# Kernel tuning notes

Hardware: AMD Instinct MI355X
Metric: run time of the kernel (lower is better)

Reference implementation:

```python
import jax, jax.numpy as jnp
import numpy as np

B, C, F = 64, 512, 48
D, H, L, HID = 16, 4, 2, 256   # d_token, n_heads, n_blocks, hidden_dim
DH = D // H
FF = 4 * D
EPS = 1e-5


def _ln(x, s, b):
    m = x.mean(-1, keepdims=True)
    v = x.var(-1, keepdims=True)
    return (x - m) * jax.lax.rsqrt(v + EPS) * s + b


def setup_inputs() -> dict:
    key = jax.random.key(0)
    ks = jax.random.split(key, 10)
    def n(k, shape, s=0.02):
        return jax.random.normal(k, shape, dtype=jnp.float32) * s
    return {
        'couple_features': jax.random.normal(ks[0], (B, F, C), dtype=jnp.float32),
        'feature_embed': n(ks[1], (F, D)),
        'feature_bias': jnp.zeros((F, D), jnp.float32),
        'cls_token': n(ks[2], (D,)),
        'track_embed': n(ks[3], (3, D)),
        'role_ids': jnp.repeat(jnp.arange(3, dtype=jnp.int32), 16),  # [0]*16+[1]*16+[2]*16
        'ln1_s': jnp.ones((L, D), jnp.float32), 'ln1_b': jnp.zeros((L, D), jnp.float32),
        'qkv_w': n(ks[4], (L, D, 3 * D), 0.1), 'qkv_b': jnp.zeros((L, 3 * D), jnp.float32),
        'out_w': n(ks[5], (L, D, D), 0.1), 'out_b': jnp.zeros((L, D), jnp.float32),
        'ln2_s': jnp.ones((L, D), jnp.float32), 'ln2_b': jnp.zeros((L, D), jnp.float32),
        'ff1_w': n(ks[6], (L, D, FF), 0.1), 'ff1_b': jnp.zeros((L, FF), jnp.float32),
        'ff2_w': n(ks[7], (L, FF, D), 0.1), 'ff2_b': jnp.zeros((L, D), jnp.float32),
        'cls2h_w': n(ks[8], (D, HID), 0.1), 'cls2h_b': jnp.zeros((HID,), jnp.float32),
    }


def reference(couple_features, feature_embed, feature_bias, cls_token, track_embed,
              role_ids, ln1_s, ln1_b, qkv_w, qkv_b, out_w, out_b,
              ln2_s, ln2_b, ff1_w, ff1_b, ff2_w, ff2_b, cls2h_w, cls2h_b):
    Bc, Fc, Cc = couple_features.shape
    N, T = Bc * Cc, Fc + 1
    # tokenise: (B,F,C) -> (B*C, F, 1) scalar * per-feature embed + bias + role embed
    scalars = couple_features.transpose(0, 2, 1).reshape(N, Fc, 1)
    tokens = scalars * feature_embed + feature_bias + track_embed[role_ids]
    cls = jnp.broadcast_to(cls_token, (N, 1, D))
    x = jnp.concatenate([cls, tokens], axis=1)  # (N, T, D)
    scale = 1.0 / np.sqrt(DH)
    for l in range(L):  # pre-LN transformer blocks (norm_first=True, gelu)
        h = _ln(x, ln1_s[l], ln1_b[l])
        qkv = h @ qkv_w[l] + qkv_b[l]
        q, k, v = jnp.split(qkv, 3, axis=-1)
        q = q.reshape(N, T, H, DH)
        k = k.reshape(N, T, H, DH)
        v = v.reshape(N, T, H, DH)
        s = jnp.einsum('nqhd,nkhd->nhqk', q, k) * scale
        a = jax.nn.softmax(s, axis=-1)
        ctx = jnp.einsum('nhqk,nkhd->nqhd', a, v).reshape(N, T, D)
        x = x + ctx @ out_w[l] + out_b[l]
        h2 = _ln(x, ln2_s[l], ln2_b[l])
        x = x + jax.nn.gelu(h2 @ ff1_w[l] + ff1_b[l], approximate=False) @ ff2_w[l] + ff2_b[l]
    cls_out = x[:, 0, :]
    out = (cls_out @ cls2h_w + cls2h_b).reshape(Bc, Cc, HID)
    return out.transpose(0, 2, 1)  # (B, hidden_dim, C)
```

## Files before the change

kernel.cpp:

```cpp
#include <hip/hip_runtime.h>
#include <math.h>

#define Bc    64
#define Cc    512
#define Fc    48
#define NTOT  32768
#define TT    49
#define NS    5
#define NBLK  ((NTOT + NS - 1) / NS)
#define QSCALE 0.72134752044448169f
#define GC1 (-2.3022082f)
#define GC2 (-0.10294324f)

#define EXP2(x) __builtin_amdgcn_exp2f(x)
#define RCP(x)  __builtin_amdgcn_rcpf(x)

using h2 = decltype(__builtin_amdgcn_cvt_pkrtz(0.f, 0.f));
typedef _Float16 f16x8 __attribute__((ext_vector_type(8)));
typedef float    f32x4 __attribute__((ext_vector_type(4)));

#define MFMA16(a,b,c) __builtin_amdgcn_mfma_f32_16x16x32_f16((a),(b),(c),0,0,0)

__device__ __forceinline__ h2 PK(float a, float b) {
    return __builtin_amdgcn_cvt_pkrtz(a, b);
}
__device__ __forceinline__ unsigned H2U(h2 h) { return __builtin_bit_cast(unsigned, h); }
__device__ __forceinline__ h2 U2H(unsigned u) { return __builtin_bit_cast(h2, u); }

__device__ __forceinline__ float DOT2(h2 a, h2 b, float c) {
#if __has_builtin(__builtin_amdgcn_fdot2)
    return __builtin_amdgcn_fdot2(a, b, c, false);
#else
    return fmaf((float)a[0], (float)b[0], fmaf((float)a[1], (float)b[1], c));
#endif
}
__device__ __forceinline__ unsigned pack_rte(float a, float b) {
    h2 h; h[0] = (_Float16)a; h[1] = (_Float16)b;
    return __builtin_bit_cast(unsigned, h);
}
__device__ __forceinline__ float gelu1(float g) {
    const float u = g * fmaf(GC2, g * g, GC1);
    return g * RCP(1.0f + EXP2(u));
}

#define OFF_QKVW 0
#define OFF_QKVB 768
#define OFF_OUTW 864
#define OFF_OUTB 1120
#define OFF_C2HW 1152
#define OFF_C2HB 3200
#define OFF_FBTE 3456
#define OFF_F1A  4224
#define OFF_F2A  6272
#define OFF_B1V  7296
#define OFF_B2V  9344
#define WS_DWORDS 9856

__global__ __launch_bounds__(256)
void pack_kernel(const float* __restrict__ qkv_w, const float* __restrict__ qkv_b,
                 const float* __restrict__ out_w, const float* __restrict__ out_b,
                 const float* __restrict__ ff1_w, const float* __restrict__ ff1_b,
                 const float* __restrict__ ff2_w, const float* __restrict__ ff2_b,
                 const float* __restrict__ c2h_w, const float* __restrict__ c2h_b,
                 const float* __restrict__ fb,    const float* __restrict__ te,
                 const int*   __restrict__ role,
                 const float* __restrict__ ln1_s, const float* __restrict__ ln1_b,
                 const float* __restrict__ ln2_s, const float* __restrict__ ln2_b,
                 unsigned* __restrict__ ws)
{
    const int gid = blockIdx.x * 256 + threadIdx.x;
    const int gs  = gridDim.x * 256;
    float* wsf = (float*)ws;
    for (int i = gid; i < 768; i += gs) {
        int dp = i & 7, jl = i >> 3, j = jl % 48, l = jl / 48;
        float w0 = qkv_w[(l*16 + 2*dp    )*48 + j] * ln1_s[l*16 + 2*dp];
        float w1 = qkv_w[(l*16 + 2*dp + 1)*48 + j] * ln1_s[l*16 + 2*dp + 1];
        if (j < 16) { w0 *= QSCALE; w1 *= QSCALE; }
        ws[OFF_QKVW + i] = pack_rte(w0, w1);
    }
    for (int i = gid; i < 96; i += gs) {
        int j = i % 48, l = i / 48;
        float a = qkv_b[i];
        for (int d = 0; d < 16; ++d) a += ln1_b[l*16+d] * qkv_w[(l*16+d)*48 + j];
        wsf[OFF_QKVB + i] = a * (j < 16 ? QSCALE : 1.0f);
    }
    for (int i = gid; i < 256; i += gs) {
        int dp = i & 7, dl = i >> 3, d = dl % 16, l = dl / 16;
        ws[OFF_OUTW + i] = pack_rte(out_w[l*256 + (2*dp)*16 + d],
                                    out_w[l*256 + (2*dp+1)*16 + d]);
    }
    for (int i = gid; i < 32; i += gs) wsf[OFF_OUTB + i] = out_b[i];
    for (int i = gid; i < 2048; i += gs) {
        int dp = i & 7, o = i >> 3;
        ws[OFF_C2HW + i] = pack_rte(c2h_w[(2*dp)*256 + o], c2h_w[(2*dp+1)*256 + o]);
    }
    for (int i = gid; i < 256; i += gs) wsf[OFF_C2HB + i] = c2h_b[i];
    for (int i = gid; i < 768; i += gs) {
        int d = i & 15, f = i >> 4;
        wsf[OFF_FBTE + i] = fb[f*16 + d] + te[role[f]*16 + d];
    }
    for (int i = gid; i < 2048; i += gs) {
        int dw = i & 3, lane = (i >> 2) & 63, mt = (i >> 8) & 3, l = i >> 10;
        int g = lane >> 4, j = 16*mt + (lane & 15);
        unsigned v = 0;
        if (g < 2) {
            int d0 = 8*g + 2*dw;
            v = pack_rte(ff1_w[l*1024 + d0*64 + j]     * ln2_s[l*16 + d0],
                         ff1_w[l*1024 + (d0+1)*64 + j] * ln2_s[l*16 + d0+1]);
        }
        ws[OFF_F1A + i] = v;
    }
    for (int i = gid; i < 1024; i += gs) {
        int dw = i & 3, lane = (i >> 2) & 63, kf = (i >> 8) & 1, l = i >> 9;
        int dim = lane & 15, j0 = 32*kf + 8*(lane >> 4) + 2*dw;
        ws[OFF_F2A + i] = pack_rte(ff2_w[l*1024 + j0*16 + dim],
                                   ff2_w[l*1024 + (j0+1)*16 + dim]);
    }
    for (int i = gid; i < 2048; i += gs) {
        int r = i & 3, lane = (i >> 2) & 63, mt = (i >> 8) & 3, l = i >> 10;
        int j = 16*mt + (lane >> 4)*4 + r;
        float a = ff1_b[l*64 + j];
        for (int d = 0; d < 16; ++d) a += ln2_b[l*16+d] * ff1_w[l*1024 + d*64 + j];
        wsf[OFF_B1V + i] = a;
    }
    for (int i = gid; i < 512; i += gs) {
        int r = i & 3, lane = (i >> 2) & 63, l = i >> 8;
        wsf[OFF_B2V + i] = ff2_b[l*16 + (lane >> 4)*4 + r];
    }
}

struct __align__(16) SeqSh {
    uint4 Kp[50][3];
    uint4 Vp[25][5];
    unsigned clsP[8];
};

__global__ __launch_bounds__(256)
void enc_kernel(const float* __restrict__ cf,  const float* __restrict__ fe,
                const float* __restrict__ cls_tok,
                const unsigned* __restrict__ wsp, float* __restrict__ out)
{
    const unsigned ut = threadIdx.x;
    const int seq = ut / 49u;
    const int row = ut - seq * 49u;
    const int n0  = blockIdx.x * NS;
    const int n   = n0 + seq;
    const bool act = (seq < NS) && (n < NTOT);
    const int b = n >> 9, c = n & 511;

    __shared__ SeqSh S[NS];
    __shared__ __align__(16) unsigned Gbuf[4 * 32 * 36];
    const float* wsf = (const float*)wsp;
    const h2 ONE = PK(1.f, 1.f);

    float x[16];
    if (act) {
        if (row == 0) {
            #pragma unroll
            for (int d = 0; d < 16; ++d) x[d] = cls_tok[d];
        } else {
            const int f = row - 1;
            const float s = cf[((long)b * Fc + f) * Cc + c];
            const float4* fep = (const float4*)(fe + f*16);
            const float4* fbp = (const float4*)(wsf + OFF_FBTE + f*16);
            #pragma unroll
            for (int j = 0; j < 4; ++j) {
                float4 e = fep[j], t4 = fbp[j];
                x[4*j+0] = fmaf(s, e.x, t4.x); x[4*j+1] = fmaf(s, e.y, t4.y);
                x[4*j+2] = fmaf(s, e.z, t4.z); x[4*j+3] = fmaf(s, e.w, t4.w);
            }
        }
    } else {
        #pragma unroll
        for (int d = 0; d < 16; ++d) x[d] = 0.f;
    }

    for (int l = 0; l < 2; ++l) {
        h2 hp[8], qp[8];
        if (act) {
            float mu = 0.f;
            #pragma unroll
            for (int d = 0; d < 16; ++d) mu += x[d];
            mu *= 0.0625f;
            float var = 0.f;
            #pragma unroll
            for (int d = 0; d < 16; ++d) { float dv = x[d]-mu; var = fmaf(dv,dv,var); }
            const float rr = rsqrtf(var*0.0625f + 1e-5f);
            const float nb = -mu * rr;
            #pragma unroll
            for (int p = 0; p < 8; ++p)
                hp[p] = PK(fmaf(x[2*p], rr, nb), fmaf(x[2*p+1], rr, nb));

            const unsigned* W = wsp + OFF_QKVW + l*384;
            const float* Bb = wsf + OFF_QKVB + l*48;
            #pragma unroll
            for (int j = 0; j < 16; j += 2) {
                float a0 = Bb[j], a1 = Bb[j+1];
                #pragma unroll
                for (int dp = 0; dp < 8; ++dp) {
                    a0 = DOT2(hp[dp], U2H(W[ j   *8+dp]), a0);
                    a1 = DOT2(hp[dp], U2H(W[(j+1)*8+dp]), a1);
                }
                qp[j>>1] = PK(a0, a1);
            }
            unsigned kdw[8];
            #pragma unroll
            for (int j = 0; j < 16; j += 2) {
                float a0 = Bb[16+j], a1 = Bb[17+j];
                #pragma unroll
                for (int dp = 0; dp < 8; ++dp) {
                    a0 = DOT2(hp[dp], U2H(W[(16+j)*8+dp]), a0);
                    a1 = DOT2(hp[dp], U2H(W[(17+j)*8+dp]), a1);
                }
                kdw[j>>1] = H2U(PK(a0, a1));
            }
            float vf[16];
            #pragma unroll
            for (int j = 0; j < 16; ++j) {
                float a = Bb[32+j];
                #pragma unroll
                for (int dp = 0; dp < 8; ++dp)
                    a = DOT2(hp[dp], U2H(W[(32+j)*8+dp]), a);
                vf[j] = a;
            }
            S[seq].Kp[row][0] = make_uint4(kdw[0],kdw[1],kdw[2],kdw[3]);
            S[seq].Kp[row][1] = make_uint4(kdw[4],kdw[5],kdw[6],kdw[7]);
            if (row < 48) {
                _Float16* vh = (_Float16*)&S[seq].Vp[row>>1][0];
                const int pr = row & 1;
                #pragma unroll
                for (int d = 0; d < 16; ++d) vh[2*d + pr] = (_Float16)vf[d];
            } else {
                unsigned* vw = (unsigned*)&S[seq].Vp[24][0];
                #pragma unroll
                for (int d = 0; d < 16; ++d) vw[d] = H2U(PK(vf[d], 0.f));
            }
            if (row == 0) {
                const uint4 z = make_uint4(0,0,0,0);
                S[seq].Kp[49][0] = z; S[seq].Kp[49][1] = z;
            }
        }
        __syncthreads();

        if (act) {
            float ctx[16];
            #pragma unroll
            for (int d = 0; d < 16; ++d) ctx[d] = 0.f;
            float ls0=0.f, ls1=0.f, ls2=0.f, ls3=0.f;
            #pragma unroll 5
            for (int kp = 0; kp < 25; ++kp) {
                const uint4 ka0 = S[seq].Kp[2*kp  ][0], ka1 = S[seq].Kp[2*kp  ][1];
                const uint4 kb0 = S[seq].Kp[2*kp+1][0], kb1 = S[seq].Kp[2*kp+1][1];
                float sa0 = DOT2(qp[0],U2H(ka0.x), DOT2(qp[1],U2H(ka0.y), 0.f));
                float sb0 = DOT2(qp[0],U2H(kb0.x), DOT2(qp[1],U2H(kb0.y), 0.f));
                float sa1 = DOT2(qp[2],U2H(ka0.z), DOT2(qp[3],U2H(ka0.w), 0.f));
                float sb1 = DOT2(qp[2],U2H(kb0.z), DOT2(qp[3],U2H(kb0.w), 0.f));
                float sa2 = DOT2(qp[4],U2H(ka1.x), DOT2(qp[5],U2H(ka1.y), 0.f));
                float sb2 = DOT2(qp[4],U2H(kb1.x), DOT2(qp[5],U2H(kb1.y), 0.f));
                float sa3 = DOT2(qp[6],U2H(ka1.z), DOT2(qp[7],U2H(ka1.w), 0.f));
                float sb3 = DOT2(qp[6],U2H(kb1.z), DOT2(qp[7],U2H(kb1.w), 0.f));
                const h2 pp0 = PK(EXP2(sa0), EXP2(sb0));
                const h2 pp1 = PK(EXP2(sa1), EXP2(sb1));
                const h2 pp2 = PK(EXP2(sa2), EXP2(sb2));
                const h2 pp3 = PK(EXP2(sa3), EXP2(sb3));
                ls0 = DOT2(pp0, ONE, ls0); ls1 = DOT2(pp1, ONE, ls1);
                ls2 = DOT2(pp2, ONE, ls2); ls3 = DOT2(pp3, ONE, ls3);
                const uint4 v0 = S[seq].Vp[kp][0], v1 = S[seq].Vp[kp][1];
                const uint4 v2 = S[seq].Vp[kp][2], v3 = S[seq].Vp[kp][3];
                ctx[ 0]=DOT2(pp0,U2H(v0.x),ctx[ 0]); ctx[ 1]=DOT2(pp0,U2H(v0.y),ctx[ 1]);
                ctx[ 2]=DOT2(pp0,U2H(v0.z),ctx[ 2]); ctx[ 3]=DOT2(pp0,U2H(v0.w),ctx[ 3]);
                ctx[ 4]=DOT2(pp1,U2H(v1.x),ctx[ 4]); ctx[ 5]=DOT2(pp1,U2H(v1.y),ctx[ 5]);
                ctx[ 6]=DOT2(pp1,U2H(v1.z),ctx[ 6]); ctx[ 7]=DOT2(pp1,U2H(v1.w),ctx[ 7]);
                ctx[ 8]=DOT2(pp2,U2H(v2.x),ctx[ 8]); ctx[ 9]=DOT2(pp2,U2H(v2.y),ctx[ 9]);
                ctx[10]=DOT2(pp2,U2H(v2.z),ctx[10]); ctx[11]=DOT2(pp2,U2H(v2.w),ctx[11]);
                ctx[12]=DOT2(pp3,U2H(v3.x),ctx[12]); ctx[13]=DOT2(pp3,U2H(v3.y),ctx[13]);
                ctx[14]=DOT2(pp3,U2H(v3.z),ctx[14]); ctx[15]=DOT2(pp3,U2H(v3.w),ctx[15]);
            }
            ls0 -= 1.f; ls1 -= 1.f; ls2 -= 1.f; ls3 -= 1.f;
            const float i0 = RCP(ls0), i1 = RCP(ls1), i2 = RCP(ls2), i3 = RCP(ls3);
            #pragma unroll
            for (int d = 0; d < 4;  ++d) ctx[d] *= i0;
            #pragma unroll
            for (int d = 4; d < 8;  ++d) ctx[d] *= i1;
            #pragma unroll
            for (int d = 8; d < 12; ++d) ctx[d] *= i2;
            #pragma unroll
            for (int d = 12; d < 16; ++d) ctx[d] *= i3;

            h2 cp[8];
            #pragma unroll
            for (int p = 0; p < 8; ++p) cp[p] = PK(ctx[2*p], ctx[2*p+1]);
            const unsigned* OW = wsp + OFF_OUTW + l*128;
            const float* OB = wsf + OFF_OUTB + l*16;
            #pragma unroll
            for (int d = 0; d < 16; ++d) {
                float a = OB[d];
                #pragma unroll
                for (int dp = 0; dp < 8; ++dp) a = DOT2(cp[dp], U2H(OW[d*8+dp]), a);
                x[d] += a;
            }
        }

        {
            float mu = 0.f;
            #pragma unroll
            for (int d = 0; d < 16; ++d) mu += x[d];
            mu *= 0.0625f;
            float var = 0.f;
            #pragma unroll
            for (int d = 0; d < 16; ++d) { float dv = x[d]-mu; var = fmaf(dv,dv,var); }
            const float rr = rsqrtf(var*0.0625f + 1e-5f);
            const float nb = -mu * rr;
            #pragma unroll
            for (int p = 0; p < 8; ++p)
                hp[p] = PK(fmaf(x[2*p], rr, nb), fmaf(x[2*p+1], rr, nb));
        }

        {
            const int L   = (int)(ut & 63u);
            const int wv  = (int)(ut >> 6u);
            const int g4  = L >> 4;
            const int l15 = L & 15;
            unsigned* Gw  = Gbuf + wv * (32*36);
            float*    Sbw = (float*)Gw;

            const uint4* f1a = (const uint4*)(wsp + OFF_F1A + l*1024);
            f16x8 A1[4];
            #pragma unroll
            for (int mt = 0; mt < 4; ++mt)
                A1[mt] = __builtin_bit_cast(f16x8, f1a[mt*64 + L]);
            const uint4* f2a = (const uint4*)(wsp + OFF_F2A + l*512);
            const f16x8 A20 = __builtin_bit_cast(f16x8, f2a[L]);
            const f16x8 A21 = __builtin_bit_cast(f16x8, f2a[64 + L]);
            const f32x4* b1p = (const f32x4*)(wsf + OFF_B1V + l*1024);
            f32x4 C1[4];
            #pragma unroll
            for (int mt = 0; mt < 4; ++mt) C1[mt] = b1p[mt*64 + L];
            const f32x4 Cb2 = ((const f32x4*)(wsf + OFF_B2V + l*256))[L];

            #pragma unroll
            for (int ct = 0; ct < 2; ++ct) {
                #pragma unroll
                for (int tt = 0; tt < 2; ++tt) {
                    const int src = 32*ct + 16*tt + l15;
                    unsigned bw0, bw1, bw2, bw3;
                    {
                        unsigned lo0 = __shfl(H2U(hp[0]), src), hh0 = __shfl(H2U(hp[4]), src);
                        unsigned lo1 = __shfl(H2U(hp[1]), src), hh1 = __shfl(H2U(hp[5]), src);
                        unsigned lo2 = __shfl(H2U(hp[2]), src), hh2 = __shfl(H2U(hp[6]), src);
                        unsigned lo3 = __shfl(H2U(hp[3]), src), hh3 = __shfl(H2U(hp[7]), src);
                        bw0 = (g4 == 0) ? lo0 : (g4 == 1) ? hh0 : 0u;
                        bw1 = (g4 == 0) ? lo1 : (g4 == 1) ? hh1 : 0u;
                        bw2 = (g4 == 0) ? lo2 : (g4 == 1) ? hh2 : 0u;
                        bw3 = (g4 == 0) ? lo3 : (g4 == 1) ? hh3 : 0u;
                    }
                    const f16x8 Bf = __builtin_bit_cast(f16x8, make_uint4(bw0, bw1, bw2, bw3));
                    #pragma unroll
                    for (int mt = 0; mt < 4; ++mt) {
                        f32x4 Dq = MFMA16(A1[mt], Bf, C1[mt]);
                        const float e0 = gelu1(Dq[0]), e1 = gelu1(Dq[1]);
                        const float e2 = gelu1(Dq[2]), e3 = gelu1(Dq[3]);
                        uint2 wv2;
                        wv2.x = H2U(PK(e0, e1));
                        wv2.y = H2U(PK(e2, e3));
                        *(uint2*)(Gw + (16*tt + l15)*36 + 8*mt + 2*g4) = wv2;
                    }
                }
                #pragma unroll
                for (int sub = 0; sub < 2; ++sub) {
                    const unsigned* gr = Gw + (16*sub + l15)*36 + 4*g4;
                    const f16x8 B0 = __builtin_bit_cast(f16x8, *(const uint4*)gr);
                    const f16x8 B1 = __builtin_bit_cast(f16x8, *(const uint4*)(gr + 16));
                    f32x4 t = MFMA16(A20, B0, Cb2);
                    t = MFMA16(A21, B1, t);
                    *(f32x4*)(Sbw + (16*sub + l15)*20 + 4*g4) = t;
                }
                if ((L >> 5) == ct) {
                    const float* sr = Sbw + (L & 31)*20;
                    #pragma unroll
                    for (int k4 = 0; k4 < 16; ++k4) x[k4] += sr[k4];
                }
            }
        }
        __syncthreads();
    }

    if (act && row == 0) {
        #pragma unroll
        for (int p = 0; p < 8; ++p) S[seq].clsP[p] = H2U(PK(x[2*p], x[2*p+1]));
    }
    __syncthreads();

    const uint4* cw = (const uint4*)(wsp + OFF_C2HW + ut*8);
    const uint4 w0 = cw[0], w1 = cw[1];
    const float bt = wsf[OFF_C2HB + ut];
    #pragma unroll
    for (int oo = 0; oo < NS; ++oo) {
        const int n2 = n0 + oo;
        if (n2 < NTOT) {
            float a = bt;
            a = DOT2(U2H(S[oo].clsP[0]), U2H(w0.x), a);
            a = DOT2(U2H(S[oo].clsP[1]), U2H(w0.y), a);
            a = DOT2(U2H(S[oo].clsP[2]), U2H(w0.z), a);
            a = DOT2(U2H(S[oo].clsP[3]), U2H(w0.w), a);
            a = DOT2(U2H(S[oo].clsP[4]), U2H(w1.x), a);
            a = DOT2(U2H(S[oo].clsP[5]), U2H(w1.y), a);
            a = DOT2(U2H(S[oo].clsP[6]), U2H(w1.z), a);
            a = DOT2(U2H(S[oo].clsP[7]), U2H(w1.w), a);
            out[((long)(n2 >> 9) * 256 + ut) * 512 + (n2 & 511)] = a;
        }
    }
}

extern "C" void kernel_launch(void* const* d_in, const int* in_sizes, int n_in,
                              void* d_out, int out_size, void* d_ws, size_t ws_size,
                              hipStream_t stream) {
    const float* cf       = (const float*)d_in[0];
    const float* fe       = (const float*)d_in[1];
    const float* fb       = (const float*)d_in[2];
    const float* cls_tok  = (const float*)d_in[3];
    const float* te       = (const float*)d_in[4];
    const int*   role_ids = (const int*)  d_in[5];
    const float* ln1_s    = (const float*)d_in[6];
    const float* ln1_b    = (const float*)d_in[7];
    const float* qkv_w    = (const float*)d_in[8];
    const float* qkv_b    = (const float*)d_in[9];
    const float* out_w    = (const float*)d_in[10];
    const float* out_b    = (const float*)d_in[11];
    const float* ln2_s    = (const float*)d_in[12];
    const float* ln2_b    = (const float*)d_in[13];
    const float* ff1_w    = (const float*)d_in[14];
    const float* ff1_b    = (const float*)d_in[15];
    const float* ff2_w    = (const float*)d_in[16];
    const float* ff2_b    = (const float*)d_in[17];
    const float* c2h_w    = (const float*)d_in[18];
    const float* c2h_b    = (const float*)d_in[19];
    float* out = (float*)d_out;
    unsigned* ws = (unsigned*)d_ws;

    pack_kernel<<<16, 256, 0, stream>>>(qkv_w, qkv_b, out_w, out_b, ff1_w, ff1_b,
                                        ff2_w, ff2_b, c2h_w, c2h_b, fb, te,
                                        role_ids, ln1_s, ln1_b, ln2_s, ln2_b, ws);
    enc_kernel<<<NBLK, 256, 0, stream>>>(cf, fe, cls_tok, ws, out);
}
```

Baseline: 417.7 us.

## Compute QKV projection with MFMA via per-wave LDS staging instead of scalar dot2

Replaces the per-thread scalar fdot2 QKV projection with 16x16x32 f16 MFMAs. The weights are prepacked into MFMA A-fragment layout and LN outputs are staged through per-wave LDS. K and V are scattered into the per-sequence shared buffers by token index, and Q is read back through LDS. The FFN input fragments now come from the same LDS staging instead of cross-lane shuffles. The attention loop peels the padded last key instead of subtracting its contribution. This removes the many scalar dot instructions per token, at the cost of extra LDS traffic, scattered half-precision stores and a changed shared-memory layout.

```diff
diff --git a/kernel.cpp b/kernel.cpp
--- a/kernel.cpp
+++ b/kernel.cpp
@@ -43,18 +43,18 @@
     return g * RCP(1.0f + EXP2(u));
 }
 
-#define OFF_QKVW 0
-#define OFF_QKVB 768
-#define OFF_OUTW 864
-#define OFF_OUTB 1120
-#define OFF_C2HW 1152
-#define OFF_C2HB 3200
-#define OFF_FBTE 3456
-#define OFF_F1A  4224
-#define OFF_F2A  6272
-#define OFF_B1V  7296
-#define OFF_B2V  9344
-#define WS_DWORDS 9856
+#define OFF_OUTW 0
+#define OFF_OUTB 256
+#define OFF_C2HW 288
+#define OFF_C2HB 2336
+#define OFF_FBTE 2592
+#define OFF_F1A  3360
+#define OFF_F2A  5408
+#define OFF_B1V  6432
+#define OFF_B2V  8480
+#define OFF_QA   8992
+#define OFF_QC   10528
+#define WS_DWORDS 12064
 
 __global__ __launch_bounds__(256)
 void pack_kernel(const float* __restrict__ qkv_w, const float* __restrict__ qkv_b,
@@ -71,19 +71,6 @@
     const int gid = blockIdx.x * 256 + threadIdx.x;
     const int gs  = gridDim.x * 256;
     float* wsf = (float*)ws;
-    for (int i = gid; i < 768; i += gs) {
-        int dp = i & 7, jl = i >> 3, j = jl % 48, l = jl / 48;
-        float w0 = qkv_w[(l*16 + 2*dp    )*48 + j] * ln1_s[l*16 + 2*dp];
-        float w1 = qkv_w[(l*16 + 2*dp + 1)*48 + j] * ln1_s[l*16 + 2*dp + 1];
-        if (j < 16) { w0 *= QSCALE; w1 *= QSCALE; }
-        ws[OFF_QKVW + i] = pack_rte(w0, w1);
-    }
-    for (int i = gid; i < 96; i += gs) {
-        int j = i % 48, l = i / 48;
-        float a = qkv_b[i];
-        for (int d = 0; d < 16; ++d) a += ln1_b[l*16+d] * qkv_w[(l*16+d)*48 + j];
-        wsf[OFF_QKVB + i] = a * (j < 16 ? QSCALE : 1.0f);
-    }
     for (int i = gid; i < 256; i += gs) {
         int dp = i & 7, dl = i >> 3, d = dl % 16, l = dl / 16;
         ws[OFF_OUTW + i] = pack_rte(out_w[l*256 + (2*dp)*16 + d],
@@ -126,6 +113,27 @@
     for (int i = gid; i < 512; i += gs) {
         int r = i & 3, lane = (i >> 2) & 63, l = i >> 8;
         wsf[OFF_B2V + i] = ff2_b[l*16 + (lane >> 4)*4 + r];
+    }
+    for (int i = gid; i < 1536; i += gs) {
+        int dw = i & 3, t = i >> 2, lane = t & 63, t2 = t >> 6, mt = t2 % 3, l = t2 / 3;
+        int g = lane >> 4, j = 16*mt + (lane & 15);
+        unsigned v = 0;
+        if (g < 2) {
+            int d0 = 8*g + 2*dw;
+            float w0 = qkv_w[(l*16+d0)*48 + j]   * ln1_s[l*16+d0];
+            float w1 = qkv_w[(l*16+d0+1)*48 + j] * ln1_s[l*16+d0+1];
+            if (mt == 0) { w0 *= QSCALE; w1 *= QSCALE; }
+            v = pack_rte(w0, w1);
+        }
+        ws[OFF_QA + i] = v;
+    }
+    for (int i = gid; i < 1536; i += gs) {
+        int r = i & 3, t = i >> 2, lane = t & 63, t2 = t >> 6, mt = t2 % 3, l = t2 / 3;
+        int j = 16*mt + (lane >> 4)*4 + r;
+        float a = qkv_b[l*48 + j];
+        for (int d = 0; d < 16; ++d) a += ln1_b[l*16+d] * qkv_w[(l*16+d)*48 + j];
+        if (mt == 0) a *= QSCALE;
+        wsf[OFF_QC + i] = a;
     }
 }
 
@@ -147,9 +155,14 @@
     const int n   = n0 + seq;
     const bool act = (seq < NS) && (n < NTOT);
     const int b = n >> 9, c = n & 511;
+    const int L = (int)(ut & 63u), wv = (int)(ut >> 6u);
+    const int g4 = L >> 4, l15 = L & 15;
 
     __shared__ SeqSh S[NS];
-    __shared__ __align__(16) unsigned Gbuf[4 * 32 * 36];
+    __shared__ __align__(16) unsigned Gbuf[4 * 1152];
+    unsigned* Gw  = Gbuf + wv * 1152;
+    unsigned* Hst = Gw;
+    unsigned* Qst = Gw + 640;
     const float* wsf = (const float*)wsp;
     const h2 ONE = PK(1.f, 1.f);
 
@@ -177,7 +190,7 @@
 
     for (int l = 0; l < 2; ++l) {
         h2 hp[8], qp[8];
-        if (act) {
+        {
             float mu = 0.f;
             #pragma unroll
             for (int d = 0; d < 16; ++d) mu += x[d];
@@ -190,54 +203,57 @@
             #pragma unroll
             for (int p = 0; p < 8; ++p)
                 hp[p] = PK(fmaf(x[2*p], rr, nb), fmaf(x[2*p+1], rr, nb));
-
-            const unsigned* W = wsp + OFF_QKVW + l*384;
-            const float* Bb = wsf + OFF_QKVB + l*48;
-            #pragma unroll
-            for (int j = 0; j < 16; j += 2) {
-                float a0 = Bb[j], a1 = Bb[j+1];
-                #pragma unroll
-                for (int dp = 0; dp < 8; ++dp) {
-                    a0 = DOT2(hp[dp], U2H(W[ j   *8+dp]), a0);
-                    a1 = DOT2(hp[dp], U2H(W[(j+1)*8+dp]), a1);
+        }
+        #pragma unroll
+        for (int j = 0; j < 4; ++j) {
+            uint2 t; t.x = H2U(hp[2*j]); t.y = H2U(hp[2*j+1]);
+            *(uint2*)(Hst + 10u*(unsigned)L + 2u*j) = t;
+        }
+        {
+            const uint4* qa  = (const uint4*)(wsp + OFF_QA + l*768);
+            const f32x4* qcf = (const f32x4*)(wsf + OFF_QC + l*768);
+            const f16x8 Aq = __builtin_bit_cast(f16x8, qa[L]);
+            const f16x8 Ak = __builtin_bit_cast(f16x8, qa[64 + L]);
+            const f16x8 Av = __builtin_bit_cast(f16x8, qa[128 + L]);
+            const f32x4 Cq = qcf[L], Ck = qcf[64 + L], Cv = qcf[128 + L];
+            #pragma unroll
+            for (int tt = 0; tt < 4; ++tt) {
+                const int trow = 16*tt + l15;
+                uint2 b0 = make_uint2(0u,0u), b1 = make_uint2(0u,0u);
+                if (g4 < 2) {
+                    b0 = *(const uint2*)(Hst + 10u*trow + 4u*g4);
+                    b1 = *(const uint2*)(Hst + 10u*trow + 4u*g4 + 2u);
                 }
-                qp[j>>1] = PK(a0, a1);
-            }
-            unsigned kdw[8];
-            #pragma unroll
-            for (int j = 0; j < 16; j += 2) {
-                float a0 = Bb[16+j], a1 = Bb[17+j];
-                #pragma unroll
-                for (int dp = 0; dp < 8; ++dp) {
-                    a0 = DOT2(hp[dp], U2H(W[(16+j)*8+dp]), a0);
-                    a1 = DOT2(hp[dp], U2H(W[(17+j)*8+dp]), a1);
+                const f16x8 Bf = __builtin_bit_cast(f16x8, make_uint4(b0.x,b0.y,b1.x,b1.y));
+                const f32x4 Dq = MFMA16(Aq, Bf, Cq);
+                const f32x4 Dk = MFMA16(Ak, Bf, Ck);
+                const f32x4 Dv = MFMA16(Av, Bf, Cv);
+                { uint2 t; t.x = H2U(PK(Dq[0],Dq[1])); t.y = H2U(PK(Dq[2],Dq[3]));
+                  *(uint2*)(Qst + 8u*trow + 2u*g4) = t; }
+                const int tok = 64*wv + trow;
+                if (tok < 245) {
+                    const int sq = (tok * 1338) >> 16;
+                    const int rw = tok - 49*sq;
+                    { uint2 t; t.x = H2U(PK(Dk[0],Dk[1])); t.y = H2U(PK(Dk[2],Dk[3]));
+                      *(uint2*)((unsigned*)&S[sq].Kp[rw][0] + 2u*g4) = t; }
+                    _Float16* vh = (_Float16*)&S[sq].Vp[rw>>1][0];
+                    const int pr = rw & 1;
+                    vh[2*(4*g4+0)+pr] = (_Float16)Dv[0];
+                    vh[2*(4*g4+1)+pr] = (_Float16)Dv[1];
+                    vh[2*(4*g4+2)+pr] = (_Float16)Dv[2];
+                    vh[2*(4*g4+3)+pr] = (_Float16)Dv[3];
+                    if (rw == 48) {
+                        vh[2*(4*g4+0)+1] = (_Float16)0.f;
+                        vh[2*(4*g4+1)+1] = (_Float16)0.f;
+                        vh[2*(4*g4+2)+1] = (_Float16)0.f;
+                        vh[2*(4*g4+3)+1] = (_Float16)0.f;
+                    }
                 }
-                kdw[j>>1] = H2U(PK(a0, a1));
-            }
-            float vf[16];
-            #pragma unroll
-            for (int j = 0; j < 16; ++j) {
-                float a = Bb[32+j];
-                #pragma unroll
-                for (int dp = 0; dp < 8; ++dp)
-                    a = DOT2(hp[dp], U2H(W[(32+j)*8+dp]), a);
-                vf[j] = a;
-            }
-            S[seq].Kp[row][0] = make_uint4(kdw[0],kdw[1],kdw[2],kdw[3]);
-            S[seq].Kp[row][1] = make_uint4(kdw[4],kdw[5],kdw[6],kdw[7]);
-            if (row < 48) {
-                _Float16* vh = (_Float16*)&S[seq].Vp[row>>1][0];
-                const int pr = row & 1;
-                #pragma unroll
-                for (int d = 0; d < 16; ++d) vh[2*d + pr] = (_Float16)vf[d];
-            } else {
-                unsigned* vw = (unsigned*)&S[seq].Vp[24][0];
-                #pragma unroll
-                for (int d = 0; d < 16; ++d) vw[d] = H2U(PK(vf[d], 0.f));
-            }
-            if (row == 0) {
-                const uint4 z = make_uint4(0,0,0,0);
-                S[seq].Kp[49][0] = z; S[seq].Kp[49][1] = z;
+            }
+            #pragma unroll
+            for (int j = 0; j < 4; ++j) {
+                uint2 t = *(const uint2*)(Qst + 8u*(unsigned)L + 2u*j);
+                qp[2*j] = U2H(t.x); qp[2*j+1] = U2H(t.y);
             }
         }
         __syncthreads();
@@ -247,8 +263,8 @@
             #pragma unroll
             for (int d = 0; d < 16; ++d) ctx[d] = 0.f;
             float ls0=0.f, ls1=0.f, ls2=0.f, ls3=0.f;
-            #pragma unroll 5
-            for (int kp = 0; kp < 25; ++kp) {
+            #pragma unroll 4
+            for (int kp = 0; kp < 24; ++kp) {
                 const uint4 ka0 = S[seq].Kp[2*kp  ][0], ka1 = S[seq].Kp[2*kp  ][1];
                 const uint4 kb0 = S[seq].Kp[2*kp+1][0], kb1 = S[seq].Kp[2*kp+1][1];
                 float sa0 = DOT2(qp[0],U2H(ka0.x), DOT2(qp[1],U2H(ka0.y), 0.f));
@@ -276,7 +292,29 @@
                 ctx[12]=DOT2(pp3,U2H(v3.x),ctx[12]); ctx[13]=DOT2(pp3,U2H(v3.y),ctx[13]);
                 ctx[14]=DOT2(pp3,U2H(v3.z),ctx[14]); ctx[15]=DOT2(pp3,U2H(v3.w),ctx[15]);
             }
-            ls0 -= 1.f; ls1 -= 1.f; ls2 -= 1.f; ls3 -= 1.f;
+            {
+                const uint4 ka0 = S[seq].Kp[48][0], ka1 = S[seq].Kp[48][1];
+                float sa0 = DOT2(qp[0],U2H(ka0.x), DOT2(qp[1],U2H(ka0.y), 0.f));
+                float sa1 = DOT2(qp[2],U2H(ka0.z), DOT2(qp[3],U2H(ka0.w), 0.f));
+                float sa2 = DOT2(qp[4],U2H(ka1.x), DOT2(qp[5],U2H(ka1.y), 0.f));
+                float sa3 = DOT2(qp[6],U2H(ka1.z), DOT2(qp[7],U2H(ka1.w), 0.f));
+                const h2 pp0 = PK(EXP2(sa0), 0.f);
+                const h2 pp1 = PK(EXP2(sa1), 0.f);
+                const h2 pp2 = PK(EXP2(sa2), 0.f);
+                const h2 pp3 = PK(EXP2(sa3), 0.f);
+                ls0 = DOT2(pp0, ONE, ls0); ls1 = DOT2(pp1, ONE, ls1);
+                ls2 = DOT2(pp2, ONE, ls2); ls3 = DOT2(pp3, ONE, ls3);
+                const uint4 v0 = S[seq].Vp[24][0], v1 = S[seq].Vp[24][1];
+                const uint4 v2 = S[seq].Vp[24][2], v3 = S[seq].Vp[24][3];
+                ctx[ 0]=DOT2(pp0,U2H(v0.x),ctx[ 0]); ctx[ 1]=DOT2(pp0,U2H(v0.y),ctx[ 1]);
+                ctx[ 2]=DOT2(pp0,U2H(v0.z),ctx[ 2]); ctx[ 3]=DOT2(pp0,U2H(v0.w),ctx[ 3]);
+                ctx[ 4]=DOT2(pp1,U2H(v1.x),ctx[ 4]); ctx[ 5]=DOT2(pp1,U2H(v1.y),ctx[ 5]);
+                ctx[ 6]=DOT2(pp1,U2H(v1.z),ctx[ 6]); ctx[ 7]=DOT2(pp1,U2H(v1.w),ctx[ 7]);
+                ctx[ 8]=DOT2(pp2,U2H(v2.x),ctx[ 8]); ctx[ 9]=DOT2(pp2,U2H(v2.y),ctx[ 9]);
+                ctx[10]=DOT2(pp2,U2H(v2.z),ctx[10]); ctx[11]=DOT2(pp2,U2H(v2.w),ctx[11]);
+                ctx[12]=DOT2(pp3,U2H(v3.x),ctx[12]); ctx[13]=DOT2(pp3,U2H(v3.y),ctx[13]);
+                ctx[14]=DOT2(pp3,U2H(v3.z),ctx[14]); ctx[15]=DOT2(pp3,U2H(v3.w),ctx[15]);
+            }
             const float i0 = RCP(ls0), i1 = RCP(ls1), i2 = RCP(ls2), i3 = RCP(ls3);
             #pragma unroll
             for (int d = 0; d < 4;  ++d) ctx[d] *= i0;
@@ -315,13 +353,24 @@
             for (int p = 0; p < 8; ++p)
                 hp[p] = PK(fmaf(x[2*p], rr, nb), fmaf(x[2*p+1], rr, nb));
         }
+        #pragma unroll
+        for (int j = 0; j < 4; ++j) {
+            uint2 t; t.x = H2U(hp[2*j]); t.y = H2U(hp[2*j+1]);
+            *(uint2*)(Hst + 10u*(unsigned)L + 2u*j) = t;
+        }
+        uint4 BfFF[4];
+        #pragma unroll
+        for (int q = 0; q < 4; ++q) {
+            uint2 b0 = make_uint2(0u,0u), b1 = make_uint2(0u,0u);
+            if (g4 < 2) {
+                b0 = *(const uint2*)(Hst + 10u*(16*q + l15) + 4u*g4);
+                b1 = *(const uint2*)(Hst + 10u*(16*q + l15) + 4u*g4 + 2u);
+            }
+            BfFF[q] = make_uint4(b0.x, b0.y, b1.x, b1.y);
+        }
 
         {
-            const int L   = (int)(ut & 63u);
-            const int wv  = (int)(ut >> 6u);
-            const int g4  = L >> 4;
-            const int l15 = L & 15;
-            unsigned* Gw  = Gbuf + wv * (32*36);
+            unsigned* Gw2 = Gw;
             float*    Sbw = (float*)Gw;
 
             const uint4* f1a = (const uint4*)(wsp + OFF_F1A + l*1024);
@@ -342,19 +391,7 @@
             for (int ct = 0; ct < 2; ++ct) {
                 #pragma unroll
                 for (int tt = 0; tt < 2; ++tt) {
-                    const int src = 32*ct + 16*tt + l15;
-                    unsigned bw0, bw1, bw2, bw3;
-                    {
-                        unsigned lo0 = __shfl(H2U(hp[0]), src), hh0 = __shfl(H2U(hp[4]), src);
-                        unsigned lo1 = __shfl(H2U(hp[1]), src), hh1 = __shfl(H2U(hp[5]), src);
-                        unsigned lo2 = __shfl(H2U(hp[2]), src), hh2 = __shfl(H2U(hp[6]), src);
-                        unsigned lo3 = __shfl(H2U(hp[3]), src), hh3 = __shfl(H2U(hp[7]), src);
-                        bw0 = (g4 == 0) ? lo0 : (g4 == 1) ? hh0 : 0u;
-                        bw1 = (g4 == 0) ? lo1 : (g4 == 1) ? hh1 : 0u;
-                        bw2 = (g4 == 0) ? lo2 : (g4 == 1) ? hh2 : 0u;
-                        bw3 = (g4 == 0) ? lo3 : (g4 == 1) ? hh3 : 0u;
-                    }
-                    const f16x8 Bf = __builtin_bit_cast(f16x8, make_uint4(bw0, bw1, bw2, bw3));
+                    const f16x8 Bf = __builtin_bit_cast(f16x8, BfFF[2*ct + tt]);
                     #pragma unroll
                     for (int mt = 0; mt < 4; ++mt) {
                         f32x4 Dq = MFMA16(A1[mt], Bf, C1[mt]);
@@ -363,12 +400,12 @@
                         uint2 wv2;
                         wv2.x = H2U(PK(e0, e1));
                         wv2.y = H2U(PK(e2, e3));
-                        *(uint2*)(Gw + (16*tt + l15)*36 + 8*mt + 2*g4) = wv2;
+                        *(uint2*)(Gw2 + (16*tt + l15)*36 + 8*mt + 2*g4) = wv2;
                     }
                 }
                 #pragma unroll
                 for (int sub = 0; sub < 2; ++sub) {
-                    const unsigned* gr = Gw + (16*sub + l15)*36 + 4*g4;
+                    const unsigned* gr = Gw2 + (16*sub + l15)*36 + 4*g4;
                     const f16x8 B0 = __builtin_bit_cast(f16x8, *(const uint4*)gr);
                     const f16x8 B1 = __builtin_bit_cast(f16x8, *(const uint4*)(gr + 16));
                     f32x4 t = MFMA16(A20, B0, Cb2);
```

Measured after the change: 392.6 us. 1.06x faster.
